# Performance work log

Measured on AMD Instinct MI355X. Metric: run time of the kernel, lower is better.

Reference implementation:

```python
import jax, jax.numpy as jnp
import numpy as np

K = 3; STRIDE = 1; PAD = 1
IN_C = 256; OUT_C = 512
SPAN = K * K * IN_C        # 2304, im2col row count
M = 3                      # ALSH augmentation dims
TABLE_SIZE = 8             # hash buckets
R = 2.5                    # LSH bin width


def setup_inputs() -> dict:
    key = jax.random.key(0)
    k1, k2, k3, k4 = jax.random.split(key, 4)
    stdv = 1.0 / np.sqrt(SPAN)
    inp = jax.random.normal(k1, (16, IN_C, 56, 56), dtype=jnp.float32)
    kernels = jax.random.uniform(k2, (OUT_C, SPAN), minval=-stdv, maxval=stdv,
                                 dtype=jnp.float32)
    a_hash = jax.random.normal(k3, (SPAN + M,), dtype=jnp.float32)
    b_hash = jax.random.uniform(k4, (1,), dtype=jnp.float32) * R
    return {"input": inp, "kernels": kernels, "a_hash": a_hash,
            "b_hash": b_hash, "mode": 1}


def _P(x, m):
    # ALSH P-augmentation: append ||x||^(2^i), i=1..m, per row. x: [O, SPAN]
    n = jnp.linalg.norm(x, axis=1, keepdims=True)
    ext = jnp.concatenate([n ** (2 ** (i + 1)) for i in range(m)], axis=1)
    return jnp.concatenate([x, ext], axis=1)  # [O, SPAN+M]


def _bucket(vals, b, r, ts):
    # floor((v+b)/r) ; fmod ts ; abs  (matches torch fmod-then-abs semantics)
    idx = jnp.floor((vals + b) / r).astype(jnp.int32)
    return jnp.abs(jnp.fmod(idx, ts))


def _im2col_matr(x):
    # [N, C, H, W] -> [SPAN, N*H2*W2]
    n = x.shape[0]
    h2 = (x.shape[2] - K + 2 * PAD) // STRIDE + 1
    w2 = (x.shape[3] - K + 2 * PAD) // STRIDE + 1
    patches = jax.lax.conv_general_dilated_patches(
        x, (K, K), (STRIDE, STRIDE), [(PAD, PAD), (PAD, PAD)])  # [N, SPAN, H2, W2]
    return patches.reshape(n, SPAN, h2 * w2).transpose(1, 0, 2).reshape(SPAN, -1), h2, w2


def reference(input, kernels, a_hash, b_hash, mode):
    n = input.shape[0]
    patch_matr, h2, w2 = _im2col_matr(input)  # [SPAN, L]

    # ---- build ALSH table: bucket of each kernel row ----
    kvals = _P(kernels, M) @ a_hash           # [OUT_C]
    kbuck = _bucket(kvals, b_hash[0], R, TABLE_SIZE)

    # ---- vote: hash every unit-normalized patch column, take modal bucket ----
    unit = patch_matr / jnp.linalg.norm(patch_matr, axis=0, keepdims=True)
    q_ext = jnp.full((M, unit.shape[1]), 0.5, dtype=unit.dtype)
    votes = a_hash @ jnp.concatenate([unit, q_ext], axis=0)  # [L]
    vbuck = _bucket(votes, b_hash[0], R, TABLE_SIZE)
    counts = jnp.bincount(vbuck, length=TABLE_SIZE)
    bucket = int(jnp.argmax(counts))

    # ---- gather active kernel rows for that bucket (data-dependent) ----
    rows = np.sort(np.where(np.asarray(kbuck) == bucket)[0])
    if rows.size != 0:
        active = kernels[jnp.asarray(rows)]          # [oc, SPAN]
        out = active @ patch_matr                    # [oc, L]
        if mode:
            out = out / (float(rows.size) / OUT_C)
        oc = int(rows.size)
    else:
        out = kernels @ patch_matr
        oc = OUT_C

    out = out.reshape(oc, n, h2 * w2).transpose(1, 0, 2).reshape(n, oc, h2, w2)
    return (out, jnp.asarray(rows, dtype=jnp.int32))
```

## Files before the change

kernel.cpp:

```cpp
#include <hip/hip_runtime.h>
#include <math.h>

#define N_    16
#define C_    256
#define H_    56
#define W_    56
#define HW_   3136
#define NPIX  50176
#define OUTC  512
#define SPAN_ 2304
#define BLKPX 256
#define HBYTES 24576
#define ZSLOT 24512
#define PXB   128
#define NPB   (NPIX / PXB)
#define NVB   (NPIX / 256)

typedef unsigned short u16;
typedef unsigned int   u32;
typedef __attribute__((ext_vector_type(8))) short bf16x8;
typedef __attribute__((ext_vector_type(8))) unsigned short u16x8;
typedef __attribute__((ext_vector_type(4))) unsigned short u16x4;
typedef __attribute__((ext_vector_type(4))) float f32x4;

__device__ __forceinline__ u16 f2bf(float v) {
    u32 x = __float_as_uint(v);
    u32 r = (x + 0x7fffu + ((x >> 16) & 1u)) >> 16;
    return (u16)r;
}

__device__ __forceinline__ int bucketf(float v, float b) {
    int idx = (int)floorf((v + b) / 2.5f);
    int r = idx % 8;
    return r < 0 ? -r : r;
}

__global__ __launch_bounds__(128) void prep2(const float* __restrict__ x,
                                             const float* __restrict__ ah,
                                             u16* __restrict__ xp,
                                             float* __restrict__ g,
                                             float* __restrict__ s2) {
    int t = threadIdx.x;
    __shared__ float aL[SPAN_];
    __shared__ u16 tl[PXB][68];
    for (int j = t; j < SPAN_; j += 128) aL[j] = ah[j];

    const int px = blockIdx.x * PXB + t;
    const int img = px / HW_;
    const size_t xbase = (size_t)img * C_ * HW_ + (px - img * HW_);

    float pg[9];
#pragma unroll
    for (int kk = 0; kk < 9; ++kk) pg[kk] = 0.f;
    float ps = 0.f;
    __syncthreads();

    for (int ph = 0; ph < 4; ++ph) {
        float R[16], Rn[16];
#pragma unroll
        for (int i = 0; i < 16; ++i)
            R[i] = x[xbase + (size_t)(ph * 64 + i) * HW_];
#pragma unroll
        for (int sub = 0; sub < 4; ++sub) {
            if (sub < 3) {
#pragma unroll
                for (int i = 0; i < 16; ++i)
                    Rn[i] = x[xbase + (size_t)(ph * 64 + (sub + 1) * 16 + i) * HW_];
            }
#pragma unroll
            for (int i = 0; i < 16; ++i) {
                int c = ph * 64 + sub * 16 + i;
                float v = R[i];
                const float* ac = &aL[c * 9];
#pragma unroll
                for (int kk = 0; kk < 9; ++kk) pg[kk] += ac[kk] * v;
                ps += v * v;
                tl[t][sub * 16 + i] = f2bf(v);
            }
            if (sub < 3) {
#pragma unroll
                for (int i = 0; i < 16; ++i) R[i] = Rn[i];
            }
        }
        __syncthreads();
        const int oct = t & 7;
#pragma unroll
        for (int pass = 0; pass < 8; ++pass) {
            int pxl = pass * 16 + (t >> 3);
            u16x8 v8 = *(const u16x8*)&tl[pxl][oct * 8];
            *(u16x8*)&xp[((size_t)(blockIdx.x * PXB + pxl)) * C_ +
                         ph * 64 + oct * 8] = v8;
        }
        __syncthreads();
    }

#pragma unroll
    for (int kk = 0; kk < 9; ++kk) g[(size_t)kk * NPIX + px] = pg[kk];
    s2[px] = ps;
}

__global__ __launch_bounds__(256) void vote_kernel(const float* __restrict__ g,
                                                   const float* __restrict__ s2,
                                                   const float* __restrict__ ah,
                                                   const float* __restrict__ bh,
                                                   const float* __restrict__ kern,
                                                   int* __restrict__ counts,
                                                   int* __restrict__ kbuck) {
    int kb = blockIdx.x - NVB;
    if (kb >= 0) {
        int wv = threadIdx.x >> 6, lane = threadIdx.x & 63;
        int oc = kb * 4 + wv;
        const float* kr = kern + (size_t)oc * SPAN_;
        float dot = 0.f, ss = 0.f;
#pragma unroll
        for (int i = 0; i < 9; ++i) {
            float4 kv = *(const float4*)(kr + i * 256 + lane * 4);
            float4 av = *(const float4*)(ah + i * 256 + lane * 4);
            dot += kv.x * av.x + kv.y * av.y + kv.z * av.z + kv.w * av.w;
            ss  += kv.x * kv.x + kv.y * kv.y + kv.z * kv.z + kv.w * kv.w;
        }
#pragma unroll
        for (int off = 32; off; off >>= 1) {
            dot += __shfl_xor(dot, off);
            ss  += __shfl_xor(ss, off);
        }
        if (lane == 0) {
            float n2 = ss;
            float n4 = n2 * n2;
            float n8 = n4 * n4;
            float v = dot + n2 * ah[SPAN_] + n4 * ah[SPAN_ + 1] +
                      n8 * ah[SPAN_ + 2];
            kbuck[oc] = bucketf(v, bh[0]);
        }
        return;
    }

    __shared__ int hist[8];
    if (threadIdx.x < 8) hist[threadIdx.x] = 0;
    __syncthreads();
    int q = blockIdx.x * 256 + threadIdx.x;
    int n = q / HW_;
    int p = q - n * HW_;
    int h = p / W_;
    int w = p - h * W_;
    float dot = 0.f, ss = 0.f;
#pragma unroll
    for (int kk = 0; kk < 9; ++kk) {
        int dh = kk / 3 - 1, dw = kk % 3 - 1;
        int hh = h + dh, ww = w + dw;
        if (hh >= 0 && hh < H_ && ww >= 0 && ww < W_) {
            int idx = n * HW_ + hh * W_ + ww;
            dot += g[(size_t)kk * NPIX + idx];
            ss  += s2[idx];
        }
    }
    float qext = 0.5f * (ah[SPAN_] + ah[SPAN_ + 1] + ah[SPAN_ + 2]);
    float v = dot / sqrtf(ss) + qext;
    int b = bucketf(v, bh[0]);
    atomicAdd(&hist[b], 1);
    __syncthreads();
    if (threadIdx.x < 8) atomicAdd(&counts[threadIdx.x], hist[threadIdx.x]);
}

__global__ __launch_bounds__(256) void prep_w(const float* __restrict__ kern,
                                              const int* __restrict__ kbuck,
                                              const int* __restrict__ counts,
                                              const int* __restrict__ mode,
                                              float* __restrict__ out,
                                              u16* __restrict__ wfrag,
                                              int nfB, int oc_total) {
    __shared__ int sc[256];
    __shared__ int rowsL[512];
    int t = threadIdx.x;
    int best = 0, bc = counts[0];
#pragma unroll
    for (int i = 1; i < 8; ++i) {
        int c = counts[i];
        if (c > bc) { bc = c; best = i; }
    }
    int f0 = (kbuck[t] == best) ? 1 : 0;
    int f1 = (kbuck[t + 256] == best) ? 1 : 0;
    sc[t] = f0 | (f1 << 16);
    __syncthreads();
    for (int off = 1; off < 256; off <<= 1) {
        int add = (t >= off) ? sc[t - off] : 0;
        __syncthreads();
        sc[t] += add;
        __syncthreads();
    }
    int tot = sc[255];
    int t0  = tot & 0xffff;
    int cnt = t0 + (tot >> 16);
    int pos0 = (sc[t] & 0xffff) - f0;
    int pos1 = t0 + (sc[t] >> 16) - f1;
    rowsL[t] = 0; rowsL[t + 256] = 0;
    __syncthreads();
    if (cnt == 0) { rowsL[t] = t; rowsL[t + 256] = t + 256; }
    else {
        if (f0) rowsL[pos0] = t;
        if (f1) rowsL[pos1] = t + 256;
    }
    __syncthreads();
    int ocEff = (cnt == 0) ? OUTC : cnt;
    float scale = (mode[0] && cnt > 0) ? 512.0f / (float)cnt : 1.0f;

    if (blockIdx.x == 0) {
        float* rout = out + (size_t)N_ * oc_total * HW_;
        int nw = ocEff < oc_total ? ocEff : oc_total;
        if (cnt == 0) {
            if (t < nw) rout[t] = (float)t;
            if (t + 256 < nw) rout[t + 256] = (float)(t + 256);
        } else {
            if (f0 && pos0 < nw) rout[pos0] = (float)t;
            if (f1 && pos1 < nw) rout[pos1] = (float)(t + 256);
        }
    }

    int e = blockIdx.x * 256 + t;
    int lane = e & 63;
    int t2 = e >> 6;
    int g = t2 % nfB;
    int s = t2 / nfB;
    int kk = s >> 3;
    int cb = s & 7;
    int q = lane >> 4;
    int mcol = lane & 15;
    int oc_i = g * 16 + mcol;
    bool valid = oc_i < ocEff;
    int row = valid ? rowsL[oc_i] : 0;
    const float* kr = kern + (size_t)row * SPAN_;
    u16 w8[8];
#pragma unroll
    for (int j = 0; j < 8; ++j) {
        int c = cb * 32 + q * 8 + j;
        float v = valid ? kr[c * 9 + kk] * scale : 0.f;
        w8[j] = f2bf(v);
    }
    u16* dst = wfrag + ((size_t)((s * nfB + g) * 64 + lane)) * 8;
#pragma unroll
    for (int j = 0; j < 8; ++j) dst[j] = w8[j];
}

__global__ __launch_bounds__(256, 2) void conv_mfma(const u16* __restrict__ xp,
                                                    const u16* __restrict__ wfrag,
                                                    float* __restrict__ out,
                                                    int nfB, int oc_total, int nby) {
    __shared__ char halo[2 * HBYTES];

    int flat = blockIdx.x;
    int bx, by;
    int full = 192 * nby;
    if (flat < full) {
        int gsz = 8 * nby;
        int gi = flat / gsz;
        int tr = flat - gi * gsz;
        by = tr >> 3;
        bx = gi * 8 + (tr & 7);
    } else {
        int tr = flat - full;
        by = tr >> 2;
        bx = 192 + (tr & 3);
    }

    const int t = threadIdx.x;
    const int lane = t & 63;
    const int wv = t >> 6;
    const int pb = bx * BLKPX;
    const int fb = by * 3;
    const int lane15 = lane & 15;
    const int laneq  = lane >> 4;

    if (t < 8) {
        int off = ((t & 4) ? HBYTES : 0) + ZSLOT + (t & 3) * 16;
        *(u16x8*)&halo[off] = (u16x8){0, 0, 0, 0, 0, 0, 0, 0};
    }

    int addrA[4][9];
#pragma unroll
    for (int f = 0; f < 4; ++f) {
        int p = pb + wv * 64 + f * 16 + lane15;
        int img = p / HW_;
        int rp = p - img * HW_;
        int h = rp / W_;
        int w = rp - h * W_;
#pragma unroll
        for (int kk = 0; kk < 9; ++kk) {
            int dh = kk / 3 - 1, dw = kk % 3 - 1;
            int hh = h + dh, ww = w + dw;
            bool val = (hh >= 0) & (hh < H_) & (ww >= 0) & (ww < W_);
            int sn = 57 + wv * 64 + f * 16 + lane15 + dw;
            int base = sn * 64 + ((laneq ^ ((sn >> 1) & 3)) << 4) - 3584;
            addrA[f][kk] = val ? base : (ZSLOT - (kk / 3) * 3584);
        }
    }

    f32x4 acc[4][3];
#pragma unroll
    for (int f = 0; f < 4; ++f)
#pragma unroll
        for (int gg = 0; gg < 3; ++gg) acc[f][gg] = (f32x4){0.f, 0.f, 0.f, 0.f};

    const char* xpb = (const char*)xp;
    const int q4 = (((t & 3) ^ ((t >> 3) & 3)) << 4);
    int gpx[6];
#pragma unroll
    for (int r = 0; r < 6; ++r) {
        int p = pb - 57 + r * 64 + (t >> 2);
        gpx[r] = p < 0 ? 0 : (p >= NPIX ? NPIX - 1 : p);
    }

#pragma unroll
    for (int r = 0; r < 6; ++r) {
        if (r < 5 || t < 252)
            __builtin_amdgcn_global_load_lds(
                (const __attribute__((address_space(1))) unsigned int*)
                    (xpb + (size_t)gpx[r] * 512 + q4),
                (__attribute__((address_space(3))) unsigned int*)
                    &halo[r * 4096 + t * 16],
                16, 0, 0);
    }

    const size_t cbStride = (size_t)nfB * 512;
    const size_t kkStride = cbStride * 8;
    const u16* wl = wfrag + (size_t)fb * 512 + (size_t)lane * 8;
    bf16x8 bB[3][3];
#define LOADB(slot, cb_, kk_) do {                                              \
    const u16* _wp = wl + (size_t)(kk_) * kkStride + (size_t)(cb_) * cbStride;  \
    _Pragma("unroll")                                                           \
    for (int _g = 0; _g < 3; ++_g)                                              \
        bB[slot][_g] = *(const bf16x8*)(_wp + (size_t)_g * 512);                \
} while (0)

    LOADB(0, 0, 0);
    LOADB(1, 0, 1);

#pragma unroll
    for (int cb = 0; cb < 8; ++cb) {
        __syncthreads();

        if (cb < 7) {
            const int nb = ((cb + 1) & 1) * HBYTES;
#pragma unroll
            for (int r = 0; r < 6; ++r) {
                if (r < 5 || t < 252)
                    __builtin_amdgcn_global_load_lds(
                        (const __attribute__((address_space(1))) unsigned int*)
                            (xpb + (size_t)gpx[r] * 512 + (cb + 1) * 64 + q4),
                        (__attribute__((address_space(3))) unsigned int*)
                            &halo[nb + r * 4096 + t * 16],
                        16, 0, 0);
            }
        }

#pragma unroll
        for (int kk = 0; kk < 9; ++kk) {
            if (kk < 7)       LOADB((kk + 2) % 3, cb, kk + 2);
            else if (cb < 7)  LOADB((kk + 2) % 3, cb + 1, kk - 7);

            const int IMM = (cb & 1) * HBYTES + (kk / 3) * 3584;
            bf16x8 aX[4];
#pragma unroll
            for (int f = 0; f < 4; ++f)
                aX[f] = *(const bf16x8*)&halo[addrA[f][kk] + IMM];
#pragma unroll
            for (int gg = 0; gg < 3; ++gg)
#pragma unroll
                for (int f = 0; f < 4; ++f)
                    acc[f][gg] = __builtin_amdgcn_mfma_f32_16x16x32_bf16(
                        aX[f], bB[kk % 3][gg], acc[f][gg], 0, 0, 0);
        }
    }
#undef LOADB

#pragma unroll
    for (int f = 0; f < 4; ++f) {
        int p0 = pb + wv * 64 + f * 16 + laneq * 4;
        int img0 = p0 / HW_;
        int hw0 = p0 - img0 * HW_;
#pragma unroll
        for (int gg = 0; gg < 3; ++gg) {
            int oc = (fb + gg) * 16 + lane15;
            if (oc < oc_total) {
                float* op = out + ((size_t)img0 * oc_total + oc) * HW_ + hw0;
                *(f32x4*)op = acc[f][gg];
            }
        }
    }
}

extern "C" void kernel_launch(void* const* d_in, const int* in_sizes, int n_in,
                              void* d_out, int out_size, void* d_ws, size_t ws_size,
                              hipStream_t stream) {
    const float* x    = (const float*)d_in[0];
    const float* kern = (const float*)d_in[1];
    const float* ah   = (const float*)d_in[2];
    const float* bh   = (const float*)d_in[3];
    const int*   mode = (const int*)d_in[4];
    float* out = (float*)d_out;

    int oc_total = (out_size % (N_ * HW_ + 1) == 0) ? out_size / (N_ * HW_ + 1)
                                                    : OUTC;
    int nfTot = (oc_total + 15) / 16;
    int nby   = (nfTot + 2) / 3;
    int nfB   = nby * 3;

    u16*   xp     = (u16*)d_ws;
    u16*   wfrag  = xp + (size_t)NPIX * C_;
    float* g      = (float*)(wfrag + (size_t)72 * 36 * 64 * 8);
    float* s2     = g + (size_t)9 * NPIX;
    int*   counts = (int*)(s2 + NPIX);
    int*   kbuck  = counts + 8;

    hipMemsetAsync(counts, 0, 8 * sizeof(int), stream);

    prep2<<<NPB, 128, 0, stream>>>(x, ah, xp, g, s2);
    vote_kernel<<<NVB + 128, 256, 0, stream>>>(g, s2, ah, bh, kern, counts,
                                               kbuck);
    prep_w<<<18 * nfB, 256, 0, stream>>>(kern, kbuck, counts, mode, out, wfrag,
                                         nfB, oc_total);
    conv_mfma<<<(NPIX / BLKPX) * nby, 256, 0, stream>>>(xp, wfrag, out, nfB,
                                                        oc_total, nby);
}
```

Before: 113.7 us.

## Halve conv block pixel tile, mask halo padding in registers, remap block order

Each block now covers 128 pixels instead of 256, so every wave handles 2 pixel fragments. The halo LDS buffer shrinks to 256 slots. Out-of-bounds taps now use a per-lane validity bitmask that selects zero in registers, replacing the precomputed per-tap addresses that pointed at a zero slot in LDS. Weight prefetch drops from a 3-slot ring to double buffering, and block indices are spread across 8 interleaved groups. Together these aim to cut register and LDS pressure and raise occupancy, at the cost of less weight reuse per block and more blocks to schedule.

```diff
diff --git a/kernel.cpp b/kernel.cpp
--- a/kernel.cpp
+++ b/kernel.cpp
@@ -9,9 +9,9 @@
 #define NPIX  50176
 #define OUTC  512
 #define SPAN_ 2304
-#define BLKPX 256
-#define HBYTES 24576
-#define ZSLOT 24512
+#define BLKPX 128
+#define HSLOTS 256
+#define HBYTES (HSLOTS * 64)
 #define PXB   128
 #define NPB   (NPIX / PXB)
 #define NVB   (NPIX / 256)
@@ -247,20 +247,12 @@
                                                     int nfB, int oc_total, int nby) {
     __shared__ char halo[2 * HBYTES];
 
-    int flat = blockIdx.x;
-    int bx, by;
-    int full = 192 * nby;
-    if (flat < full) {
-        int gsz = 8 * nby;
-        int gi = flat / gsz;
-        int tr = flat - gi * gsz;
-        by = tr >> 3;
-        bx = gi * 8 + (tr & 7);
-    } else {
-        int tr = flat - full;
-        by = tr >> 2;
-        bx = 192 + (tr & 3);
-    }
+    const int tot = (NPIX / BLKPX) * nby;
+    const int q8 = tot >> 3;
+    const int flat = blockIdx.x;
+    const int virt = (flat & 7) * q8 + (flat >> 3);
+    const int bx = virt / nby;
+    const int by = virt - bx * nby;
 
     const int t = threadIdx.x;
     const int lane = t & 63;
@@ -270,48 +262,49 @@
     const int lane15 = lane & 15;
     const int laneq  = lane >> 4;
 
-    if (t < 8) {
-        int off = ((t & 4) ? HBYTES : 0) + ZSLOT + (t & 3) * 16;
-        *(u16x8*)&halo[off] = (u16x8){0, 0, 0, 0, 0, 0, 0, 0};
-    }
-
-    int addrA[4][9];
-#pragma unroll
-    for (int f = 0; f < 4; ++f) {
-        int p = pb + wv * 64 + f * 16 + lane15;
+    u32 valMask[2];
+    int aB[2][3];
+#pragma unroll
+    for (int f = 0; f < 2; ++f) {
+        int p = pb + wv * 32 + f * 16 + lane15;
         int img = p / HW_;
         int rp = p - img * HW_;
         int h = rp / W_;
         int w = rp - h * W_;
+        u32 m = 0;
 #pragma unroll
         for (int kk = 0; kk < 9; ++kk) {
             int dh = kk / 3 - 1, dw = kk % 3 - 1;
             int hh = h + dh, ww = w + dw;
-            bool val = (hh >= 0) & (hh < H_) & (ww >= 0) & (ww < W_);
-            int sn = 57 + wv * 64 + f * 16 + lane15 + dw;
-            int base = sn * 64 + ((laneq ^ ((sn >> 1) & 3)) << 4) - 3584;
-            addrA[f][kk] = val ? base : (ZSLOT - (kk / 3) * 3584);
-        }
-    }
-
-    f32x4 acc[4][3];
-#pragma unroll
-    for (int f = 0; f < 4; ++f)
+            if (hh >= 0 && hh < H_ && ww >= 0 && ww < W_) m |= (1u << kk);
+        }
+        valMask[f] = m;
+#pragma unroll
+        for (int j = 0; j < 3; ++j) {
+            int sn = 57 + wv * 32 + f * 16 + lane15 + (j - 1);
+            aB[f][j] = sn * 64 + ((laneq ^ ((sn >> 1) & 3)) << 4) - 3584;
+        }
+    }
+
+    f32x4 acc[2][3];
+#pragma unroll
+    for (int f = 0; f < 2; ++f)
 #pragma unroll
         for (int gg = 0; gg < 3; ++gg) acc[f][gg] = (f32x4){0.f, 0.f, 0.f, 0.f};
+    const bf16x8 zf = {0, 0, 0, 0, 0, 0, 0, 0};
 
     const char* xpb = (const char*)xp;
     const int q4 = (((t & 3) ^ ((t >> 3) & 3)) << 4);
-    int gpx[6];
-#pragma unroll
-    for (int r = 0; r < 6; ++r) {
+    int gpx[4];
+#pragma unroll
+    for (int r = 0; r < 4; ++r) {
         int p = pb - 57 + r * 64 + (t >> 2);
         gpx[r] = p < 0 ? 0 : (p >= NPIX ? NPIX - 1 : p);
     }
 
 #pragma unroll
-    for (int r = 0; r < 6; ++r) {
-        if (r < 5 || t < 252)
+    for (int r = 0; r < 4; ++r) {
+        if (r < 3 || t < 200)
             __builtin_amdgcn_global_load_lds(
                 (const __attribute__((address_space(1))) unsigned int*)
                     (xpb + (size_t)gpx[r] * 512 + q4),
@@ -323,16 +316,15 @@
     const size_t cbStride = (size_t)nfB * 512;
     const size_t kkStride = cbStride * 8;
     const u16* wl = wfrag + (size_t)fb * 512 + (size_t)lane * 8;
-    bf16x8 bB[3][3];
-#define LOADB(slot, cb_, kk_) do {                                              \
+    bf16x8 bW[3], bWn[3];
+#define LOADB(dst, cb_, kk_) do {                                               \
     const u16* _wp = wl + (size_t)(kk_) * kkStride + (size_t)(cb_) * cbStride;  \
     _Pragma("unroll")                                                           \
     for (int _g = 0; _g < 3; ++_g)                                              \
-        bB[slot][_g] = *(const bf16x8*)(_wp + (size_t)_g * 512);                \
+        dst[_g] = *(const bf16x8*)(_wp + (size_t)_g * 512);                     \
 } while (0)
 
-    LOADB(0, 0, 0);
-    LOADB(1, 0, 1);
+    LOADB(bW, 0, 0);
 
 #pragma unroll
     for (int cb = 0; cb < 8; ++cb) {
@@ -341,8 +333,8 @@
         if (cb < 7) {
             const int nb = ((cb + 1) & 1) * HBYTES;
 #pragma unroll
-            for (int r = 0; r < 6; ++r) {
-                if (r < 5 || t < 252)
+            for (int r = 0; r < 4; ++r) {
+                if (r < 3 || t < 200)
                     __builtin_amdgcn_global_load_lds(
                         (const __attribute__((address_space(1))) unsigned int*)
                             (xpb + (size_t)gpx[r] * 512 + (cb + 1) * 64 + q4),
@@ -354,27 +346,35 @@
 
 #pragma unroll
         for (int kk = 0; kk < 9; ++kk) {
-            if (kk < 7)       LOADB((kk + 2) % 3, cb, kk + 2);
-            else if (cb < 7)  LOADB((kk + 2) % 3, cb + 1, kk - 7);
-
-            const int IMM = (cb & 1) * HBYTES + (kk / 3) * 3584;
-            bf16x8 aX[4];
-#pragma unroll
-            for (int f = 0; f < 4; ++f)
-                aX[f] = *(const bf16x8*)&halo[addrA[f][kk] + IMM];
+            if (kk < 8)       LOADB(bWn, cb, kk + 1);
+            else if (cb < 7)  LOADB(bWn, cb + 1, 0);
+
+            const int dh = kk / 3 - 1;
+            const int j  = kk % 3;
+            const int IMM = (cb & 1) * HBYTES + (dh + 1) * 3584;
+            bf16x8 aX[2];
+#pragma unroll
+            for (int f = 0; f < 2; ++f) {
+                bf16x8 a = *(const bf16x8*)&halo[aB[f][j] + IMM];
+                aX[f] = ((valMask[f] >> kk) & 1) ? a : zf;
+            }
 #pragma unroll
             for (int gg = 0; gg < 3; ++gg)
 #pragma unroll
-                for (int f = 0; f < 4; ++f)
+                for (int f = 0; f < 2; ++f)
                     acc[f][gg] = __builtin_amdgcn_mfma_f32_16x16x32_bf16(
-                        aX[f], bB[kk % 3][gg], acc[f][gg], 0, 0, 0);
+                        aX[f], bW[gg], acc[f][gg], 0, 0, 0);
+            if (kk < 8 || cb < 7) {
+#pragma unroll
+                for (int gg = 0; gg < 3; ++gg) bW[gg] = bWn[gg];
+            }
         }
     }
 #undef LOADB
 
 #pragma unroll
-    for (int f = 0; f < 4; ++f) {
-        int p0 = pb + wv * 64 + f * 16 + laneq * 4;
+    for (int f = 0; f < 2; ++f) {
+        int p0 = pb + wv * 32 + f * 16 + laneq * 4;
         int img0 = p0 / HW_;
         int hw0 = p0 - img0 * HW_;
 #pragma unroll
```

After: 98.72 us. 13.2% less time.
